# Kernel tuning notes

Measured on AMD Instinct MI355X. Metric: run time of the kernel, lower is better.

## Reference

```python
import jax, jax.numpy as jnp
import numpy as np

C = 32          # in/out channels per spnn.Conv3d(32, 32, 2, stride=2)
KVOL = 8        # 2^3 kernel offsets
GRID = 128      # voxel grid resolution
N_RAW = 1_000_000


def setup_inputs() -> dict:
    rng = np.random.default_rng(0)
    # unique active voxel coordinates (torchsparse coords are unique)
    coords = np.unique(rng.integers(0, GRID, size=(N_RAW, 3), dtype=np.int32), axis=0)
    n = coords.shape[0]
    # kernel=2, stride=2: each input voxel hits exactly one output voxel
    out_coords = coords // 2
    k_idx = (coords[:, 0] % 2) * 4 + (coords[:, 1] % 2) * 2 + (coords[:, 2] % 2)
    _, out_idx = np.unique(out_coords, axis=0, return_inverse=True)
    num_out = int(out_idx.max()) + 1

    key = jax.random.key(0)
    kx, kw = jax.random.split(key)
    x = jax.random.normal(kx, (n, C), dtype=jnp.float32)
    W = jax.random.normal(kw, (KVOL, C, C), dtype=jnp.float32) * 0.05
    return {
        "x": x,
        "W": W,
        "k_idx": jnp.asarray(k_idx, dtype=jnp.int32),
        "out_idx": jnp.asarray(out_idx, dtype=jnp.int32),
        "num_out": num_out,
    }


def reference(x, W, k_idx, out_idx, num_out):
    # gather -> per-offset GEMM -> scatter-add (sparse conv kernel-map form)
    # proj[n, k, d] = sum_c x[n, c] * W[k, c, d]
    proj = jnp.einsum("nc,kcd->nkd", x, W)
    # pick the projection for each point's kernel offset: [n, C]
    sel = jnp.take_along_axis(proj, k_idx[:, None, None], axis=1)[:, 0, :]
    # scatter-add into output voxels
    out = jax.ops.segment_sum(sel, out_idx, num_segments=num_out)
    return out
```

## Files before the change

kernel.cpp:

```cpp
#include <hip/hip_runtime.h>
#include <hip/hip_bf16.h>


typedef __attribute__((ext_vector_type(8))) short bf16x8;
typedef __attribute__((ext_vector_type(4))) float f32x4;

union ABFrag { bf16x8 v; int i[4]; };

__device__ __forceinline__ unsigned short f2bf(float f) {
    union { float f; unsigned u; } v; v.f = f;
    unsigned r = v.u + 0x7FFFu + ((v.u >> 16) & 1u);
    return (unsigned short)(r >> 16);
}

__global__ __launch_bounds__(256) void prep_and_map_kernel(
    const float* __restrict__ W, unsigned short* __restrict__ WB,
    const int* __restrict__ k_idx, const int* __restrict__ out_idx,
    int* __restrict__ child, int n)
{
    int t = blockIdx.x * blockDim.x + threadIdx.x;
    if (t < 8 * 2 * 64 * 8) {
        int j    = t & 7;
        int lane = (t >> 3) & 63;
        int half = (t >> 9) & 1;
        int k    = t >> 10;
        int c = (lane >> 4) * 8 + j;
        int d = half * 16 + (lane & 15);
        WB[t] = f2bf(W[k * 1024 + c * 32 + d]);
    }
    if (t < n) child[(size_t)out_idx[t] * 8 + k_idx[t]] = t;
}

__global__ __launch_bounds__(256) void conv_gather_kernel(
    const float* __restrict__ x,
    const unsigned short* __restrict__ WB,
    const int* __restrict__ child,
    float* __restrict__ out,
    int num_out)
{
    const int lane  = threadIdx.x & 63;
    const int wv    = threadIdx.x >> 6;
    const int obase = (blockIdx.x * 4 + wv) * 16;
    if (obase >= num_out) return;

    const int row  = lane & 15;
    const int quad = lane >> 4;
    const int o = obase + row;

    int4 c0 = make_int4(-1, -1, -1, -1), c1 = make_int4(-1, -1, -1, -1);
    if (o < num_out) {
        const int4* cp = (const int4*)(child + (size_t)o * 8);
        c0 = cp[0]; c1 = cp[1];
    }
    int pk[8] = {c0.x, c0.y, c0.z, c0.w, c1.x, c1.y, c1.z, c1.w};

    float4 xa[8], xb[8];
#pragma unroll
    for (int k = 0; k < 8; ++k) {
        xa[k] = make_float4(0.f, 0.f, 0.f, 0.f);
        xb[k] = make_float4(0.f, 0.f, 0.f, 0.f);
        if (pk[k] >= 0) {
            const float* xp = x + (size_t)pk[k] * 32 + quad * 8;
            xa[k] = *(const float4*)xp;
            xb[k] = *(const float4*)(xp + 4);
        }
    }

    f32x4 acc0 = {0.f, 0.f, 0.f, 0.f};
    f32x4 acc1 = {0.f, 0.f, 0.f, 0.f};

#pragma unroll
    for (int k = 0; k < 8; ++k) {
        ABFrag a;
        a.i[0] = (int)f2bf(xa[k].x) | ((int)f2bf(xa[k].y) << 16);
        a.i[1] = (int)f2bf(xa[k].z) | ((int)f2bf(xa[k].w) << 16);
        a.i[2] = (int)f2bf(xb[k].x) | ((int)f2bf(xb[k].y) << 16);
        a.i[3] = (int)f2bf(xb[k].z) | ((int)f2bf(xb[k].w) << 16);
        bf16x8 b0 = *(const bf16x8*)(WB + ((size_t)(k * 2 + 0) * 64 + lane) * 8);
        bf16x8 b1 = *(const bf16x8*)(WB + ((size_t)(k * 2 + 1) * 64 + lane) * 8);
        acc0 = __builtin_amdgcn_mfma_f32_16x16x32_bf16(a.v, b0, acc0, 0, 0, 0);
        acc1 = __builtin_amdgcn_mfma_f32_16x16x32_bf16(a.v, b1, acc1, 0, 0, 0);
    }

#pragma unroll
    for (int r = 0; r < 4; ++r) {
        int oo = obase + quad * 4 + r;
        if (oo < num_out) {
            float* op = out + (size_t)oo * 32 + (lane & 15);
            __builtin_nontemporal_store(acc0[r], op);
            __builtin_nontemporal_store(acc1[r], op + 16);
        }
    }
}

__global__ __launch_bounds__(256) void conv_atomic_kernel(
    const float* __restrict__ x, const unsigned short* __restrict__ WB,
    const int* __restrict__ k_idx, const int* __restrict__ out_idx,
    float* __restrict__ out, int n)
{
    const int lane = threadIdx.x & 63;
    const int wv   = threadIdx.x >> 6;
    const int base = (blockIdx.x * 4 + wv) * 16;
    if (base >= n) return;
    const int row = lane & 15, quad = lane >> 4;
    const int p = base + row;
    int krow = -1;
    ABFrag a; a.i[0] = a.i[1] = a.i[2] = a.i[3] = 0;
    if (p < n) {
        krow = k_idx[p];
        const float* xp = x + (size_t)p * 32 + quad * 8;
        float4 x0 = *(const float4*)xp;
        float4 x1 = *(const float4*)(xp + 4);
        a.i[0] = (int)f2bf(x0.x) | ((int)f2bf(x0.y) << 16);
        a.i[1] = (int)f2bf(x0.z) | ((int)f2bf(x0.w) << 16);
        a.i[2] = (int)f2bf(x1.x) | ((int)f2bf(x1.y) << 16);
        a.i[3] = (int)f2bf(x1.z) | ((int)f2bf(x1.w) << 16);
    }
    f32x4 acc0 = {0.f,0.f,0.f,0.f}, acc1 = {0.f,0.f,0.f,0.f};
#pragma unroll
    for (int k = 0; k < 8; ++k) {
        bf16x8 b0 = *(const bf16x8*)(WB + ((size_t)(k*2+0)*64 + lane)*8);
        bf16x8 b1 = *(const bf16x8*)(WB + ((size_t)(k*2+1)*64 + lane)*8);
        const bool keep = (krow == k);
        ABFrag ak;
        ak.i[0] = keep ? a.i[0] : 0; ak.i[1] = keep ? a.i[1] : 0;
        ak.i[2] = keep ? a.i[2] : 0; ak.i[3] = keep ? a.i[3] : 0;
        acc0 = __builtin_amdgcn_mfma_f32_16x16x32_bf16(ak.v, b0, acc0, 0, 0, 0);
        acc1 = __builtin_amdgcn_mfma_f32_16x16x32_bf16(ak.v, b1, acc1, 0, 0, 0);
    }
#pragma unroll
    for (int r = 0; r < 4; ++r) {
        int p2 = base + quad * 4 + r;
        if (p2 < n) {
            int oi = out_idx[p2];
            float* op = out + (size_t)oi * 32 + (lane & 15);
            atomicAdd(op,      acc0[r]);
            atomicAdd(op + 16, acc1[r]);
        }
    }
}

extern "C" void kernel_launch(void* const* d_in, const int* in_sizes, int n_in,
                              void* d_out, int out_size, void* d_ws, size_t ws_size,
                              hipStream_t stream) {
    const float* x       = (const float*)d_in[0];
    const float* W       = (const float*)d_in[1];
    const int*   k_idx   = (const int*)d_in[2];
    const int*   out_idx = (const int*)d_in[3];
    const int n = in_sizes[2];
    const int num_out = out_size / 32;
    float* out = (float*)d_out;

    unsigned short* WB = (unsigned short*)d_ws;
    const size_t wb_bytes = 16384;
    int* child = (int*)((char*)d_ws + wb_bytes);
    const size_t child_bytes = (size_t)num_out * 8 * sizeof(int);

    if (ws_size >= wb_bytes + child_bytes) {
        hipMemsetAsync(child, 0xFF, child_bytes, stream);
        int total = n > 8192 ? n : 8192;
        prep_and_map_kernel<<<(total + 255) / 256, 256, 0, stream>>>(
            W, WB, k_idx, out_idx, child, n);
        int blocks = (num_out + 63) / 64;
        conv_gather_kernel<<<blocks, 256, 0, stream>>>(x, WB, child, out, num_out);
    } else {
        prep_and_map_kernel<<<32, 256, 0, stream>>>(W, WB, k_idx, out_idx,
                                                    (int*)nullptr, 0);
        hipMemsetAsync(d_out, 0, (size_t)out_size * sizeof(float), stream);
        int blocks = (n + 63) / 64;
        conv_atomic_kernel<<<blocks, 256, 0, stream>>>(x, WB, k_idx, out_idx, out, n);
    }
}
```

Before: 178.3 us.

## Make gather conv a persistent-wave kernel with double-buffered tile prefetch

Replaces the one-tile-per-wave gather kernel with a persistent grid capped at 2048 waves. Each wave loops over tiles and prefetches the next tile's child indices and x rows into a second register set while computing the current tile. Loads become unconditional, clamped to row 0 and masked afterwards, and the bf16 packing uses the hardware pair-conversion intrinsic. This is meant to hide gather latency and cut launch overhead, but it doubles register use per wave and may lower occupancy.

Result: slower. 187.4 us (+5.1%).

```diff
diff --git a/kernel.cpp b/kernel.cpp
--- a/kernel.cpp
+++ b/kernel.cpp
@@ -11,6 +11,12 @@
     union { float f; unsigned u; } v; v.f = f;
     unsigned r = v.u + 0x7FFFu + ((v.u >> 16) & 1u);
     return (unsigned short)(r >> 16);
+}
+
+__device__ __forceinline__ int packbf2(float lo, float hi) {
+    union { __hip_bfloat162 h; int i; } u;
+    u.h = __float22bfloat162_rn(make_float2(lo, hi));
+    return u.i;
 }
 
 __global__ __launch_bounds__(256) void prep_and_map_kernel(
@@ -31,66 +37,85 @@
     if (t < n) child[(size_t)out_idx[t] * 8 + k_idx[t]] = t;
 }
 
-__global__ __launch_bounds__(256) void conv_gather_kernel(
+__global__ __launch_bounds__(256) void conv_pipe_kernel(
     const float* __restrict__ x,
     const unsigned short* __restrict__ WB,
     const int* __restrict__ child,
     float* __restrict__ out,
-    int num_out)
+    int num_out, int nwaves)
 {
-    const int lane  = threadIdx.x & 63;
-    const int wv    = threadIdx.x >> 6;
-    const int obase = (blockIdx.x * 4 + wv) * 16;
-    if (obase >= num_out) return;
-
+    const int lane = threadIdx.x & 63;
+    const int wid  = blockIdx.x * 4 + (threadIdx.x >> 6);
     const int row  = lane & 15;
     const int quad = lane >> 4;
-    const int o = obase + row;
-
-    int4 c0 = make_int4(-1, -1, -1, -1), c1 = make_int4(-1, -1, -1, -1);
-    if (o < num_out) {
-        const int4* cp = (const int4*)(child + (size_t)o * 8);
-        c0 = cp[0]; c1 = cp[1];
-    }
-    int pk[8] = {c0.x, c0.y, c0.z, c0.w, c1.x, c1.y, c1.z, c1.w};
-
-    float4 xa[8], xb[8];
-#pragma unroll
-    for (int k = 0; k < 8; ++k) {
-        xa[k] = make_float4(0.f, 0.f, 0.f, 0.f);
-        xb[k] = make_float4(0.f, 0.f, 0.f, 0.f);
-        if (pk[k] >= 0) {
-            const float* xp = x + (size_t)pk[k] * 32 + quad * 8;
-            xa[k] = *(const float4*)xp;
-            xb[k] = *(const float4*)(xp + 4);
-        }
-    }
-
-    f32x4 acc0 = {0.f, 0.f, 0.f, 0.f};
-    f32x4 acc1 = {0.f, 0.f, 0.f, 0.f};
-
-#pragma unroll
-    for (int k = 0; k < 8; ++k) {
-        ABFrag a;
-        a.i[0] = (int)f2bf(xa[k].x) | ((int)f2bf(xa[k].y) << 16);
-        a.i[1] = (int)f2bf(xa[k].z) | ((int)f2bf(xa[k].w) << 16);
-        a.i[2] = (int)f2bf(xb[k].x) | ((int)f2bf(xb[k].y) << 16);
-        a.i[3] = (int)f2bf(xb[k].z) | ((int)f2bf(xb[k].w) << 16);
-        bf16x8 b0 = *(const bf16x8*)(WB + ((size_t)(k * 2 + 0) * 64 + lane) * 8);
-        bf16x8 b1 = *(const bf16x8*)(WB + ((size_t)(k * 2 + 1) * 64 + lane) * 8);
-        acc0 = __builtin_amdgcn_mfma_f32_16x16x32_bf16(a.v, b0, acc0, 0, 0, 0);
-        acc1 = __builtin_amdgcn_mfma_f32_16x16x32_bf16(a.v, b1, acc1, 0, 0, 0);
-    }
-
-#pragma unroll
-    for (int r = 0; r < 4; ++r) {
-        int oo = obase + quad * 4 + r;
-        if (oo < num_out) {
-            float* op = out + (size_t)oo * 32 + (lane & 15);
-            __builtin_nontemporal_store(acc0[r], op);
-            __builtin_nontemporal_store(acc1[r], op + 16);
-        }
-    }
+    const int ntiles = (num_out + 15) >> 4;
+
+    int tA = wid;
+    if (tA >= ntiles) return;
+
+    int pkA[8]; f32x4 xaA[8], xbA[8];
+    int pkB[8]; f32x4 xaB[8], xbB[8];
+
+#define LOADT(pk_, xa_, xb_, t_)                                              \
+    {                                                                         \
+        int o = (t_) * 16 + row;                                              \
+        int4 c0 = make_int4(-1, -1, -1, -1), c1 = make_int4(-1, -1, -1, -1);  \
+        if (o < num_out) {                                                    \
+            const int4* cp = (const int4*)(child + (size_t)o * 8);            \
+            c0 = cp[0]; c1 = cp[1];                                           \
+        }                                                                     \
+        pk_[0] = c0.x; pk_[1] = c0.y; pk_[2] = c0.z; pk_[3] = c0.w;           \
+        pk_[4] = c1.x; pk_[5] = c1.y; pk_[6] = c1.z; pk_[7] = c1.w;           \
+        _Pragma("unroll")                                                     \
+        for (int k = 0; k < 8; ++k) {                                         \
+            int pc = pk_[k] >= 0 ? pk_[k] : 0;                                \
+            const f32x4* xp = (const f32x4*)(x + (size_t)pc * 32 + quad * 8); \
+            xa_[k] = xp[0]; xb_[k] = xp[1];                                   \
+        }                                                                     \
+    }
+
+#define COMPT(pk_, xa_, xb_, t_)                                              \
+    {                                                                         \
+        f32x4 acc0 = {0.f, 0.f, 0.f, 0.f};                                    \
+        f32x4 acc1 = {0.f, 0.f, 0.f, 0.f};                                    \
+        _Pragma("unroll")                                                     \
+        for (int k = 0; k < 8; ++k) {                                         \
+            const int m = (pk_[k] >= 0) ? -1 : 0;                             \
+            ABFrag a;                                                         \
+            a.i[0] = packbf2(xa_[k][0], xa_[k][1]) & m;                       \
+            a.i[1] = packbf2(xa_[k][2], xa_[k][3]) & m;                       \
+            a.i[2] = packbf2(xb_[k][0], xb_[k][1]) & m;                       \
+            a.i[3] = packbf2(xb_[k][2], xb_[k][3]) & m;                       \
+            bf16x8 b0 = *(const bf16x8*)(WB + ((size_t)(k*2+0)*64 + lane)*8); \
+            bf16x8 b1 = *(const bf16x8*)(WB + ((size_t)(k*2+1)*64 + lane)*8); \
+            acc0 = __builtin_amdgcn_mfma_f32_16x16x32_bf16(a.v, b0, acc0, 0, 0, 0); \
+            acc1 = __builtin_amdgcn_mfma_f32_16x16x32_bf16(a.v, b1, acc1, 0, 0, 0); \
+        }                                                                     \
+        _Pragma("unroll")                                                     \
+        for (int r = 0; r < 4; ++r) {                                         \
+            int oo = (t_) * 16 + quad * 4 + r;                                \
+            if (oo < num_out) {                                               \
+                float* op = out + (size_t)oo * 32 + row;                      \
+                __builtin_nontemporal_store(acc0[r], op);                     \
+                __builtin_nontemporal_store(acc1[r], op + 16);                \
+            }                                                                 \
+        }                                                                     \
+    }
+
+    LOADT(pkA, xaA, xbA, tA);
+    while (true) {
+        int tB = tA + nwaves;
+        if (tB < ntiles) LOADT(pkB, xaB, xbB, tB);
+        COMPT(pkA, xaA, xbA, tA);
+        if (tB >= ntiles) break;
+        int tC = tB + nwaves;
+        if (tC < ntiles) LOADT(pkA, xaA, xbA, tC);
+        COMPT(pkB, xaB, xbB, tB);
+        if (tC >= ntiles) break;
+        tA = tC;
+    }
+#undef LOADT
+#undef COMPT
 }
 
 __global__ __launch_bounds__(256) void conv_atomic_kernel(
@@ -157,16 +182,19 @@
     const size_t child_bytes = (size_t)num_out * 8 * sizeof(int);
 
     if (ws_size >= wb_bytes + child_bytes) {
-        hipMemsetAsync(child, 0xFF, child_bytes, stream);
+        (void)hipMemsetAsync(child, 0xFF, child_bytes, stream);
         int total = n > 8192 ? n : 8192;
         prep_and_map_kernel<<<(total + 255) / 256, 256, 0, stream>>>(
             W, WB, k_idx, out_idx, child, n);
-        int blocks = (num_out + 63) / 64;
-        conv_gather_kernel<<<blocks, 256, 0, stream>>>(x, WB, child, out, num_out);
+        int ntiles = (num_out + 15) / 16;
+        int nwaves = ntiles < 2048 ? ntiles : 2048;
+        int blocks = (nwaves + 3) / 4;
+        conv_pipe_kernel<<<blocks, 256, 0, stream>>>(
+            x, WB, child, out, num_out, blocks * 4);
     } else {
         prep_and_map_kernel<<<32, 256, 0, stream>>>(W, WB, k_idx, out_idx,
                                                     (int*)nullptr, 0);
-        hipMemsetAsync(d_out, 0, (size_t)out_size * sizeof(float), stream);
+        (void)hipMemsetAsync(d_out, 0, (size_t)out_size * sizeof(float), stream);
         int blocks = (n + 63) / 64;
         conv_atomic_kernel<<<blocks, 256, 0, stream>>>(x, WB, k_idx, out_idx, out, n);
     }
```
